# Performance work log

Hardware: AMD Instinct MI355X
Metric: run time of the kernel (lower is better)

Reference implementation:

```python
import jax, jax.numpy as jnp
import numpy as np

N, E, D, R, B = 30000, 100000, 200, 100, 50
BN_EPS = 1e-5


def setup_inputs() -> dict:
    key = jax.random.key(0)
    ks = list(jax.random.split(key, 26))
    s = 1.0 / np.sqrt(D)  # xavier-ish scale
    lin = lambda k: jax.random.normal(k, (D, D), jnp.float32) * s
    bias = lambda k: jax.random.normal(k, (D,), jnp.float32) * 0.01
    return {
        "n_in_feats": jax.random.normal(ks[0], (N, D), jnp.float32),
        "r_feats": jax.random.normal(ks[1], (R, D), jnp.float32),
        "norm": jax.random.uniform(ks[2], (E, 1), jnp.float32),
        "loop_rel": jax.random.normal(ks[3], (1, D), jnp.float32) * s,
        "relation_att": jax.random.normal(ks[4], (B, D, D), jnp.float32) * s,
        "w_comp": jax.random.normal(ks[5], (R, B), jnp.float32) * 0.115,
        "wO_w": lin(ks[6]), "wO_b": bias(ks[7]),
        "wI_w": lin(ks[8]), "wI_b": bias(ks[9]),
        "wS_w": lin(ks[10]), "wS_b": bias(ks[11]),
        "wR_w": lin(ks[12]), "wR_b": bias(ks[13]),
        "k_w": lin(ks[14]), "k_b": bias(ks[15]),
        "q_w": lin(ks[16]), "q_b": bias(ks[17]),
        "v_w": lin(ks[18]), "v_b": bias(ks[19]),
        "bn_gamma": jnp.ones((D,), jnp.float32),
        "bn_beta": jnp.zeros((D,), jnp.float32),
        "src": jax.random.randint(ks[20], (E,), 0, N),
        "dst": jax.random.randint(ks[21], (E,), 0, N),
        "etype": jax.random.randint(ks[22], (E,), 0, R),
        "in_mask": jax.random.randint(ks[23], (E,), 0, 2, dtype=jnp.int32),
    }


def reference(n_in_feats, r_feats, norm, loop_rel, relation_att, w_comp,
              wO_w, wO_b, wI_w, wI_b, wS_w, wS_b, wR_w, wR_b,
              k_w, k_b, q_w, q_b, v_w, v_b, bn_gamma, bn_beta,
              src, dst, etype, in_mask):
    r_all = jnp.concatenate([r_feats, loop_rel], axis=0)      # [R+1, D]
    x_src = n_in_feats[src]                                   # [E, D]
    x_dst = n_in_feats[dst]                                   # [E, D]

    # composition (comp_fn='sub') + in/out projections.
    # NOTE: in the original source new_comp_h is computed and stored on edges
    # but never consumed downstream (dead w.r.t. outputs); kept for fidelity.
    comp_h = x_src - r_all[etype] * norm                      # [E, D]
    new_comp_h = jnp.where(in_mask[:, None] > 0,
                           comp_h @ wI_w.T + wI_b,
                           comp_h @ wO_w.T + wO_b)            # [E, D] (unused)

    # per-edge k/q/v from endpoint node features
    k = x_src @ k_w.T + k_b                                   # [E, D]
    q = x_dst @ q_w.T + q_b                                   # [E, D]
    v = x_src @ v_w.T + v_b                                   # [E, D]

    # basis-decomposed relational attention: att_e = k_e^T (sum_b w_comp[t_e,b] A_b) q_e
    # scan over bases avoids materializing [E, B, D]
    def per_basis(c, A_b):
        return c, jnp.sum((k @ A_b) * q, axis=-1)             # [E]
    _, s = jax.lax.scan(per_basis, None, relation_att)        # [B, E]
    att = jnp.sum(w_comp[etype] * s.T, axis=-1)               # [E]

    # segment softmax over destination nodes (== DGL mailbox softmax)
    m = jax.ops.segment_max(att, dst, num_segments=N)
    m = jnp.where(jnp.isfinite(m), m, 0.0)                    # empty segments -> 0
    ex = jnp.exp(att - m[dst])
    denom = jax.ops.segment_sum(ex, dst, num_segments=N)
    wts = ex / jnp.maximum(denom[dst], 1e-30)                 # [E]
    agg = jax.ops.segment_sum(wts[:, None] * v, dst, num_segments=N)  # [N, D]

    # self-loop branch + merge (dropout is identity at eval)
    comp_h_s = n_in_feats - loop_rel                          # sub with loop relation
    n_out = ((comp_h_s @ wS_w.T + wS_b) + agg) * (1.0 / 3.0)

    # BatchNorm1d in training mode (batch statistics, biased variance)
    mean = jnp.mean(n_out, axis=0)
    var = jnp.var(n_out, axis=0)
    n_out = bn_gamma * (n_out - mean) * jax.lax.rsqrt(var + BN_EPS) + bn_beta
    n_out = jnp.tanh(n_out)

    r_out = (r_all @ wR_w.T + wR_b)[:-1]                      # [R, D]
    return n_out, r_out
```

## Files before the change

### kernel.cpp

```cpp
#include <hip/hip_runtime.h>
#include <hip/hip_bf16.h>
#include <math.h>

typedef __hip_bfloat16 bf16;
typedef __attribute__((ext_vector_type(8))) short short8;
typedef __attribute__((ext_vector_type(4))) float f32x4;

#define NN 30000
#define NE 100000
#define DD 200
#define NR 100
#define NB 50
#define NDIM (NN*DD)
#define MAXCH 1664
#define NBLK 391
#define SEGB 40

#define KP 224
#define NCOLP 896
#define MIP 208

#define O_K      0
#define O_V      6240000
#define O_QH     12240000
#define O_QL     15600000
#define O_MH     18960000
#define O_ML     21289600
#define O_WTH    23619200
#define O_WTL    23719552
#define O_B800   23819904
#define O_ATT    23820704
#define O_SUM    23920704
#define O_SSQ    23920904
#define O_CNT    23921104
#define O_OFFS   23921204
#define O_CUR    23921305
#define O_CHOFF  23921405
#define O_NCH    23921506
#define O_CHT    23921507
#define O_CHS    23923171
#define O_CHL    23924835
#define O_EIDX   23926499
#define O_CNTD   24026499
#define O_OFFD   24056499
#define O_CURD   24086500
#define O_EIDXD  24116500
#define O_BH     24216500

__device__ __forceinline__ float cvt(float x) { return x; }
__device__ __forceinline__ float cvt(bf16 x) { return __bfloat162float(x); }
__device__ __forceinline__ short f2bf(float f) {
    union { float f; unsigned u; } x; x.f = f;
    unsigned r = x.u + 0x7FFFu + ((x.u >> 16) & 1u);
    return (short)(r >> 16);
}
__device__ __forceinline__ float bf2f(short b) {
    union { unsigned u; float f; } x; x.u = ((unsigned)(unsigned short)b) << 16;
    return x.f;
}
__device__ __forceinline__ bool bfmode(const void* gam) {
    return *(const unsigned*)gam != 0x3F800000u;
}

__global__ void k_init(float* __restrict__ ws) {
    int g = blockIdx.x * 256 + threadIdx.x;
    int* wi = (int*)ws;
    if (g < NN) wi[O_CNTD + g] = 0;
    if (g < DD) { ws[O_SUM + g] = 0.f; ws[O_SSQ + g] = 0.f; }
}

template <typename T>
__device__ __forceinline__ void prep_body(float* __restrict__ ws,
        const T* kw, const T* qw, const T* vw, const T* sw,
        const T* kb, const T* qb, const T* vb, const T* sb, const T* lr, int g) {
    if (g < NCOLP * KP) {
        int c = g / KP, k = g % KP;
        float val = 0.f;
        if (c < 800 && k < DD) {
            int m = c / 200, cc = c - m * 200;
            const T* w = (m == 0) ? kw : (m == 1) ? qw : (m == 2) ? vw : sw;
            val = cvt(w[cc * 200 + k]);
        }
        short hi = f2bf(val);
        short lo = f2bf(val - bf2f(hi));
        ((short*)(ws + O_WTH))[g] = hi;
        ((short*)(ws + O_WTL))[g] = lo;
    } else if (g < NCOLP * KP + 800) {
        int c = g - NCOLP * KP;
        int m = c / 200, cc = c - m * 200;
        float v;
        if (m == 0) v = cvt(kb[cc]);
        else if (m == 1) v = cvt(qb[cc]);
        else if (m == 2) v = cvt(vb[cc]);
        else {
            float acc = cvt(sb[cc]);
            for (int j = 0; j < DD; j++) acc -= cvt(lr[j]) * cvt(sw[cc * 200 + j]);
            v = acc;
        }
        ws[O_B800 + c] = v;
    }
}
__global__ void k_prep(float* __restrict__ ws,
                       const void* kw, const void* qw, const void* vw, const void* sw,
                       const void* kb, const void* qb, const void* vb, const void* sb,
                       const void* lr, const void* gam) {
    int g = blockIdx.x * 256 + threadIdx.x;
    if (bfmode(gam))
        prep_body(ws, (const bf16*)kw, (const bf16*)qw, (const bf16*)vw, (const bf16*)sw,
                  (const bf16*)kb, (const bf16*)qb, (const bf16*)vb, (const bf16*)sb,
                  (const bf16*)lr, g);
    else
        prep_body(ws, (const float*)kw, (const float*)qw, (const float*)vw, (const float*)sw,
                  (const float*)kb, (const float*)qb, (const float*)vb, (const float*)sb,
                  (const float*)lr, g);
}

template <typename T>
__device__ __forceinline__ void compmt_body(float* __restrict__ ws, const T* A, const T* wc,
                                            float* wl, int tid, int bx, int by) {
    for (int idx = tid; idx < NR * NB; idx += 256) wl[idx] = cvt(wc[idx]);
    __syncthreads();
    int x = bx * 256 + tid;
    int i = x / KP, j = x - i * KP;
    bool valid = (i < DD) && (j < DD);
    float a[NB];
    if (valid) {
        #pragma unroll
        for (int b = 0; b < NB; b++) a[b] = cvt(A[b * 40000 + i * 200 + j]);
    } else {
        #pragma unroll
        for (int b = 0; b < NB; b++) a[b] = 0.f;
    }
    short* mh = (short*)(ws + O_MH);
    short* ml = (short*)(ws + O_ML);
    int t0 = by * 25;
    for (int t = t0; t < t0 + 25; t++) {
        float acc = 0.f;
        #pragma unroll
        for (int b = 0; b < NB; b++) acc = fmaf(wl[t * NB + b], a[b], acc);
        short hi = f2bf(acc);
        short lo = f2bf(acc - bf2f(hi));
        mh[(size_t)t * (MIP * KP) + x] = hi;
        ml[(size_t)t * (MIP * KP) + x] = lo;
    }
}
__global__ void k_compmt(float* __restrict__ ws, const void* A, const void* wc,
                         const void* gam) {
    __shared__ float wl[NR * NB];
    if (bfmode(gam)) compmt_body(ws, (const bf16*)A, (const bf16*)wc, wl,
                                 threadIdx.x, blockIdx.x, blockIdx.y);
    else             compmt_body(ws, (const float*)A, (const float*)wc, wl,
                                 threadIdx.x, blockIdx.x, blockIdx.y);
}

__global__ void k_hist(float* __restrict__ ws, const int* __restrict__ ety,
                       const int* __restrict__ dst) {
    __shared__ int lh[NR];
    int tid = threadIdx.x;
    if (tid < NR) lh[tid] = 0;
    __syncthreads();
    int e = blockIdx.x * 256 + tid;
    int* wi = (int*)ws;
    if (e < NE) {
        atomicAdd(&lh[ety[e]], 1);
        atomicAdd(&wi[O_CNTD + dst[e]], 1);
    }
    __syncthreads();
    if (tid < NR) wi[O_BH + blockIdx.x * NR + tid] = lh[tid];
}

__global__ void k_scans(float* __restrict__ ws) {
    __shared__ int part[1024];
    __shared__ int segsum[10 * NR];
    __shared__ int cntL[NR];
    __shared__ int offsL[NR + 1];
    int* wi = (int*)ws;
    int tid = threadIdx.x;
    int t = tid % NR, seg = tid / NR;

    if (tid < 1000) {
        int b0 = seg * SEGB;
        int b1 = min(NBLK, b0 + SEGB);
        int s = 0;
        for (int b = b0; b < b1; b++) s += wi[O_BH + b * NR + t];
        segsum[seg * NR + t] = s;
    }
    __syncthreads();
    if (tid < NR) {
        int s = 0;
        #pragma unroll
        for (int g = 0; g < 10; g++) s += segsum[g * NR + tid];
        cntL[tid] = s;
        wi[O_CNT + tid] = s;
    }
    __syncthreads();
    if (tid == 0) {
        int run = 0, chrun = 0;
        for (int ty = 0; ty < NR; ty++) {
            offsL[ty] = run;
            wi[O_OFFS + ty] = run;
            wi[O_CHOFF + ty] = chrun;
            run += cntL[ty];
            chrun += (cntL[ty] + 63) >> 6;
        }
        offsL[NR] = run;
        wi[O_OFFS + NR] = run;
        wi[O_CHOFF + NR] = chrun;
        wi[O_NCH] = chrun;
    }
    __syncthreads();
    if (tid < 1000) {
        int base = offsL[t];
        for (int g = 0; g < seg; g++) base += segsum[g * NR + t];
        int b0 = seg * SEGB;
        int nb = min(NBLK - b0, SEGB);
        int cvals[SEGB];
        #pragma unroll
        for (int i = 0; i < SEGB; i++)
            if (i < nb) cvals[i] = wi[O_BH + (b0 + i) * NR + t];
        #pragma unroll
        for (int i = 0; i < SEGB; i++) {
            if (i < nb) {
                wi[O_BH + (b0 + i) * NR + t] = base;
                base += cvals[i];
            }
        }
    }
    __syncthreads();
    int nch = wi[O_NCH];
    for (int c = tid; c < nch; c += 1024) {
        int lo = 0, hi = NR;
        while (hi - lo > 1) {
            int mid = (lo + hi) >> 1;
            if (wi[O_CHOFF + mid] <= c) lo = mid; else hi = mid;
        }
        int local = c - wi[O_CHOFF + lo];
        wi[O_CHT + c] = lo;
        wi[O_CHS + c] = offsL[lo] + local * 64;
        wi[O_CHL + c] = min(64, cntL[lo] - local * 64);
    }
    __syncthreads();
    int i0 = tid * 30;
    int s = 0;
    for (int u = 0; u < 30; u++) { int i = i0 + u; if (i < NN) s += wi[O_CNTD + i]; }
    part[tid] = s;
    __syncthreads();
    for (int off = 1; off < 1024; off <<= 1) {
        int v = 0;
        if (tid >= off) v = part[tid - off];
        __syncthreads();
        part[tid] += v;
        __syncthreads();
    }
    int run = part[tid] - s;
    for (int u = 0; u < 30; u++) {
        int i = i0 + u;
        if (i < NN) {
            wi[O_OFFD + i] = run;
            wi[O_CURD + i] = run;
            run += wi[O_CNTD + i];
        }
    }
    if (tid == 1023) wi[O_OFFD + NN] = part[1023];
}

__global__ void k_scatter(float* __restrict__ ws, const int* __restrict__ ety,
                          const int* __restrict__ dst) {
    __shared__ int lcnt[NR];
    int tid = threadIdx.x;
    if (tid < NR) lcnt[tid] = 0;
    __syncthreads();
    int e = blockIdx.x * 256 + tid;
    int* wi = (int*)ws;
    if (e < NE) {
        int t = ety[e];
        int r = atomicAdd(&lcnt[t], 1);
        wi[O_EIDX + wi[O_BH + blockIdx.x * NR + t] + r] = e;
        int p2 = atomicAdd(&wi[O_CURD + dst[e]], 1);
        wi[O_EIDXD + p2] = e;
    }
}

__global__ __launch_bounds__(256, 3) void k_ngemm(float* __restrict__ ws, const float* __restrict__ X,
                                                  float* __restrict__ outAgg) {
    __shared__ short Bh[128 * 40];
    __shared__ short Bl[128 * 40];
    int tid = threadIdx.x;
    int wid = tid >> 6, lane = tid & 63;
    int l16 = lane & 15, quad = lane >> 4;
    int r0 = blockIdx.x * 64 + wid * 16;
    int c0 = blockIdx.y * 128;
    bool needLo = (c0 < 400);

    const float* xr = X + (size_t)min(r0 + l16, NN - 1) * DD;
    short8 ah[7], al[7];
    #pragma unroll
    for (int kk = 0; kk < 7; kk++) {
        int k0 = kk * 32 + quad * 8;
        float v[8] = {0.f, 0.f, 0.f, 0.f, 0.f, 0.f, 0.f, 0.f};
        if (k0 < DD) {
            float4 v0 = *(const float4*)(xr + k0);
            float4 v1 = *(const float4*)(xr + k0 + 4);
            v[0] = v0.x; v[1] = v0.y; v[2] = v0.z; v[3] = v0.w;
            v[4] = v1.x; v[5] = v1.y; v[6] = v1.z; v[7] = v1.w;
        }
        #pragma unroll
        for (int j = 0; j < 8; j++) {
            short hi = f2bf(v[j]);
            ah[kk][j] = hi;
            al[kk][j] = f2bf(v[j] - bf2f(hi));
        }
    }

    const short* WTH = (const short*)(ws + O_WTH);
    const short* WTL = (const short*)(ws + O_WTL);
    f32x4 acc[8] = {};
    for (int kk = 0; kk < 7; kk++) {
        {
            int n = tid >> 1;
            int ko = (tid & 1) * 16;
            size_t off = (size_t)(c0 + n) * KP + kk * 32 + ko;
            *(float4*)&Bh[n * 40 + ko]     = *(const float4*)(WTH + off);
            *(float4*)&Bh[n * 40 + ko + 8] = *(const float4*)(WTH + off + 8);
            if (needLo) {
                *(float4*)&Bl[n * 40 + ko]     = *(const float4*)(WTL + off);
                *(float4*)&Bl[n * 40 + ko + 8] = *(const float4*)(WTL + off + 8);
            }
        }
        __syncthreads();
        #pragma unroll
        for (int nt = 0; nt < 8; nt++) {
            int ro = (nt * 16 + l16) * 40 + quad * 8;
            short8 bh = *(const short8*)&Bh[ro];
            acc[nt] = __builtin_amdgcn_mfma_f32_16x16x32_bf16(ah[kk], bh, acc[nt], 0, 0, 0);
            acc[nt] = __builtin_amdgcn_mfma_f32_16x16x32_bf16(al[kk], bh, acc[nt], 0, 0, 0);
            if (c0 + nt * 16 < 400) {
                short8 bl = *(const short8*)&Bl[ro];
                acc[nt] = __builtin_amdgcn_mfma_f32_16x16x32_bf16(ah[kk], bl, acc[nt], 0, 0, 0);
            }
        }
        __syncthreads();
    }

    const float* B800 = ws + O_B800;
    short* QHs = (short*)(ws + O_QH);
    short* QLs = (short*)(ws + O_QL);
    float* Kp = ws + O_K;
    short* VpS = (short*)(ws + O_V);
    int rowBase = r0 + quad * 4;
    #pragma unroll
    for (int nt = 0; nt < 8; nt++) {
        int col = c0 + nt * 16 + l16;
        if (col < 800) {
            int m = (col >= 600) ? 3 : (col >= 400) ? 2 : (col >= 200) ? 1 : 0;
            int cc = col - m * 200;
            float bias = B800[col];
            #pragma unroll
            for (int reg = 0; reg < 4; reg++) {
                int row = rowBase + reg;
                if (row >= NN) continue;
                float v = acc[nt][reg] + bias;
                if (m == 0) Kp[(size_t)row * 208 + cc] = v;
                else if (m == 1) {
                    short hi = f2bf(v);
                    short lo = f2bf(v - bf2f(hi));
                    QHs[(size_t)row * 224 + cc] = hi;
                    QLs[(size_t)row * 224 + cc] = lo;
                } else if (m == 2) VpS[(size_t)row * 200 + cc] = f2bf(v);
                else outAgg[(size_t)row * 200 + cc] = v;
            }
        } else {
            int p = col - 800;
            #pragma unroll
            for (int reg = 0; reg < 4; reg++) {
                int row = rowBase + reg;
                if (row >= NN) continue;
                if (p < 8)        Kp[(size_t)row * 208 + 200 + p] = 0.f;
                else if (p < 32)  QHs[(size_t)row * 224 + 192 + p] = 0;
                else if (p < 56)  QLs[(size_t)row * 224 + 168 + p] = 0;
            }
        }
    }
}

template <int MTN>
__device__ __forceinline__ void attn_core(
        const short* (&qh)[4], const short* (&ql)[4],
        const short* mhb, const short* mlb,
        const float* __restrict__ Kp, const int* __restrict__ srcv, const int (&eId)[4],
        int mt0, int quad, float (&part)[4]) {
    f32x4 acc[4][MTN];
    #pragma unroll
    for (int et = 0; et < 4; et++)
        #pragma unroll
        for (int ml = 0; ml < MTN; ml++) acc[et][ml] = (f32x4){0.f, 0.f, 0.f, 0.f};

    #pragma unroll
    for (int kc = 0; kc < 7; kc++) {
        int kk = kc * 32;
        short8 bh[4], bl[4];
        #pragma unroll
        for (int et = 0; et < 4; et++) {
            bh[et] = *(const short8*)(qh[et] + kk);
            bl[et] = *(const short8*)(ql[et] + kk);
        }
        #pragma unroll
        for (int ml = 0; ml < MTN; ml++) {
            short8 ah = *(const short8*)(mhb + (size_t)ml * 16 * KP + kk);
            short8 al = *(const short8*)(mlb + (size_t)ml * 16 * KP + kk);
            #pragma unroll
            for (int et = 0; et < 4; et++) {
                acc[et][ml] = __builtin_amdgcn_mfma_f32_16x16x32_bf16(ah, bh[et], acc[et][ml], 0, 0, 0);
                acc[et][ml] = __builtin_amdgcn_mfma_f32_16x16x32_bf16(ah, bl[et], acc[et][ml], 0, 0, 0);
                acc[et][ml] = __builtin_amdgcn_mfma_f32_16x16x32_bf16(al, bh[et], acc[et][ml], 0, 0, 0);
            }
        }
    }

    #pragma unroll
    for (int et = 0; et < 4; et++) {
        const float* krow = Kp + (size_t)srcv[eId[et]] * 208 + mt0 * 16 + quad * 4;
        float p = 0.f;
        #pragma unroll
        for (int ml = 0; ml < MTN; ml++) {
            float4 kv = *(const float4*)(krow + ml * 16);
            p = fmaf(kv.x, acc[et][ml][0], p);
            p = fmaf(kv.y, acc[et][ml][1], p);
            p = fmaf(kv.z, acc[et][ml][2], p);
            p = fmaf(kv.w, acc[et][ml][3], p);
        }
        part[et] = p;
    }
}

__global__ __launch_bounds__(256) void k_attn(const int* __restrict__ cht, const int* __restrict__ chs,
                                              const int* __restrict__ chl, const int* __restrict__ nchp,
                                              const int* __restrict__ eidx, const int* __restrict__ srcv,
                                              const int* __restrict__ dstv,
                                              const float* __restrict__ Kp,
                                              const short* __restrict__ QH, const short* __restrict__ QL,
                                              const short* __restrict__ MH, const short* __restrict__ ML,
                                              float* __restrict__ attOut) {
    __shared__ float attp[4 * 64];
    int b = blockIdx.x;
    int b2 = (b & 7) * 208 + (b >> 3);
    if (b2 >= nchp[0]) return;
    int tid = threadIdx.x;
    int wid = tid >> 6, lane = tid & 63;
    int l16 = lane & 15, quad = lane >> 4;
    int t   = __builtin_amdgcn_readfirstlane(cht[b2]);
    int s0  = __builtin_amdgcn_readfirstlane(chs[b2]);
    int len = __builtin_amdgcn_readfirstlane(chl[b2]);
    int mt0 = wid * 3;

    int eId[4];
    const short* qh[4];
    const short* ql[4];
    #pragma unroll
    for (int et = 0; et < 4; et++) {
        eId[et] = eidx[s0 + min(et * 16 + l16, len - 1)];
        int dn = dstv[eId[et]];
        qh[et] = QH + (size_t)dn * KP + quad * 8;
        ql[et] = QL + (size_t)dn * KP + quad * 8;
    }
    const short* mhb = MH + (size_t)t * (MIP * KP) + (size_t)(mt0 * 16 + l16) * KP + quad * 8;
    const short* mlb = ML + (size_t)t * (MIP * KP) + (size_t)(mt0 * 16 + l16) * KP + quad * 8;

    float part[4];
    if (wid == 3) attn_core<4>(qh, ql, mhb, mlb, Kp, srcv, eId, mt0, quad, part);
    else          attn_core<3>(qh, ql, mhb, mlb, Kp, srcv, eId, mt0, quad, part);

    #pragma unroll
    for (int et = 0; et < 4; et++) {
        float v = part[et];
        v += __shfl_xor(v, 16);
        v += __shfl_xor(v, 32);
        if (quad == 0) attp[wid * 64 + et * 16 + l16] = v;
    }
    __syncthreads();
    if (tid < 64 && tid < len) {
        attOut[eidx[s0 + tid]] = attp[tid] + attp[64 + tid] + attp[128 + tid] + attp[192 + tid];
    }
}

__global__ __launch_bounds__(256) void k_nodeagg(const int* __restrict__ offd, const int* __restrict__ eidxd,
                                                 const int* __restrict__ src, const float* __restrict__ att,
                                                 const short* __restrict__ V, float* __restrict__ agg) {
    int wav = threadIdx.x >> 6, lane = threadIdx.x & 63;
    int n = blockIdx.x * 4 + wav;
    if (n >= NN) return;
    int o0 = offd[n], o1 = offd[n + 1];
    float* arow = agg + (size_t)n * 200;
    if (o1 > o0) {
        float a0 = arow[lane], a1 = arow[64 + lane], a2 = arow[128 + lane];
        float a3 = (lane < 8) ? arow[192 + lane] : 0.f;
        float m = -INFINITY;
        for (int p = o0; p < o1; p++) m = fmaxf(m, att[eidxd[p]]);
        float den = 0.f;
        for (int p = o0; p < o1; p++) den += expf(att[eidxd[p]] - m);
        float rden = 1.f / fmaxf(den, 1e-30f);
        for (int p = o0; p < o1; p++) {
            int e = eidxd[p];
            float w = expf(att[e] - m) * rden;
            const short* vrow = V + (size_t)src[e] * 200;
            a0 = fmaf(w, bf2f(vrow[lane]), a0);
            a1 = fmaf(w, bf2f(vrow[64 + lane]), a1);
            a2 = fmaf(w, bf2f(vrow[128 + lane]), a2);
            if (lane < 8) a3 = fmaf(w, bf2f(vrow[192 + lane]), a3);
        }
        arow[lane] = a0; arow[64 + lane] = a1; arow[128 + lane] = a2;
        if (lane < 8) arow[192 + lane] = a3;
    }
}

__global__ void k_bnstats(const float* __restrict__ agg, float* __restrict__ sum,
                          float* __restrict__ ssq) {
    int col = threadIdx.x;
    if (col >= DD) return;
    int r0 = blockIdx.x * 120;
    float s = 0.f, q = 0.f;
    for (int r = 0; r < 120; r++) {
        float x = agg[(size_t)(r0 + r) * 200 + col] * (1.f / 3.f);
        s += x;
        q = fmaf(x, x, q);
    }
    atomicAdd(&sum[col], s);
    atomicAdd(&ssq[col], q);
}

template <typename T>
__device__ __forceinline__ void bnfin_body(float* sum, float* ssq, const T* gamma, const T* beta, int d) {
    float mean = sum[d] * (1.f / NN);
    float var = ssq[d] * (1.f / NN) - mean * mean;
    float inv = rsqrtf(var + 1e-5f);
    float scale = cvt(gamma[d]) * inv;
    float shift = cvt(beta[d]) - mean * scale;
    sum[d] = scale;
    ssq[d] = shift;
}
__global__ void k_bnfin(float* __restrict__ sum, float* __restrict__ ssq,
                        const void* gamma, const void* beta) {
    int d = threadIdx.x;
    if (d >= DD) return;
    if (bfmode(gamma)) bnfin_body(sum, ssq, (const bf16*)gamma, (const bf16*)beta, d);
    else               bnfin_body(sum, ssq, (const float*)gamma, (const float*)beta, d);
}

template <typename T>
__device__ __forceinline__ void rout_body(const T* rf, const T* wr, const T* wrb,
                                          float* out, int g) {
    int r = g / 200, d = g - r * 200;
    float acc = cvt(wrb[d]);
    const T* xr = rf + r * 200;
    const T* wrow = wr + d * 200;
    for (int k = 0; k < 200; k++) acc = fmaf(cvt(xr[k]), cvt(wrow[k]), acc);
    out[NDIM + g] = acc;
}
__global__ void k_finish(const float* __restrict__ agg, const float* __restrict__ scale,
                         const float* __restrict__ shift,
                         const void* rf, const void* wr, const void* wrb,
                         float* __restrict__ out, const void* gam) {
    int bx = blockIdx.x;
    if (bx < 23438) {
        int g = bx * 256 + threadIdx.x;
        if (g >= NDIM) return;
        int d = g % 200;
        float x = agg[g] * (1.f / 3.f);
        float y = fmaf(x, scale[d], shift[d]);
        out[g] = tanhf(y);
    } else {
        int g = (bx - 23438) * 256 + threadIdx.x;
        if (g >= NR * DD) return;
        if (bfmode(gam)) rout_body((const bf16*)rf, (const bf16*)wr, (const bf16*)wrb, out, g);
        else             rout_body((const float*)rf, (const float*)wr, (const float*)wrb, out, g);
    }
}

extern "C" void kernel_launch(void* const* d_in, const int* in_sizes, int n_in,
                              void* d_out, int out_size, void* d_ws, size_t ws_size,
                              hipStream_t stream) {
    (void)in_sizes; (void)n_in; (void)out_size; (void)ws_size;
    const void* X   = d_in[0];
    const void* RF  = d_in[1];
    const void* LR  = d_in[3];
    const void* A   = d_in[4];
    const void* WC  = d_in[5];
    const void* SW  = d_in[10]; const void* SB = d_in[11];
    const void* RW  = d_in[12]; const void* RB = d_in[13];
    const void* KW  = d_in[14]; const void* KB = d_in[15];
    const void* QW  = d_in[16]; const void* QB = d_in[17];
    const void* VW  = d_in[18]; const void* VB = d_in[19];
    const void* GAM = d_in[20]; const void* BET = d_in[21];
    const int* src = (const int*)d_in[22];
    const int* dst = (const int*)d_in[23];
    const int* ety = (const int*)d_in[24];
    float* ws = (float*)d_ws;
    int* wsi = (int*)d_ws;
    float* out = (float*)d_out;

    k_init<<<118, 256, 0, stream>>>(ws);
    k_prep<<<788, 256, 0, stream>>>(ws, KW, QW, VW, SW, KB, QB, VB, SB, LR, GAM);
    k_compmt<<<dim3(182, 4), 256, 0, stream>>>(ws, A, WC, GAM);
    k_hist<<<NBLK, 256, 0, stream>>>(ws, ety, dst);
    k_scans<<<1, 1024, 0, stream>>>(ws);
    k_scatter<<<NBLK, 256, 0, stream>>>(ws, ety, dst);
    k_ngemm<<<dim3(469, 7), 256, 0, stream>>>(ws, (const float*)X, out);
    k_attn<<<MAXCH, 256, 0, stream>>>(wsi + O_CHT, wsi + O_CHS, wsi + O_CHL, wsi + O_NCH,
                                      wsi + O_EIDX, src, dst,
                                      ws + O_K,
                                      (const short*)(ws + O_QH), (const short*)(ws + O_QL),
                                      (const short*)(ws + O_MH), (const short*)(ws + O_ML),
                                      ws + O_ATT);
    k_nodeagg<<<7500, 256, 0, stream>>>(wsi + O_OFFD, wsi + O_EIDXD, src,
                                        ws + O_ATT, (const short*)(ws + O_V), out);
    k_bnstats<<<250, 256, 0, stream>>>(out, ws + O_SUM, ws + O_SSQ);
    k_bnfin<<<1, 256, 0, stream>>>(ws + O_SUM, ws + O_SSQ, GAM, BET);
    k_finish<<<23517, 256, 0, stream>>>(out, ws + O_SUM, ws + O_SSQ, RF, RW, RB, out, GAM);
}
```

Before: 473.3 us.

## Interleave hi/lo bf16 planes, fuse setup kernels, dst-ordered attention buffers

```diff
diff --git a/kernel.cpp b/kernel.cpp
--- a/kernel.cpp
+++ b/kernel.cpp
@@ -19,33 +19,32 @@
 #define KP 224
 #define NCOLP 896
 #define MIP 208
+#define MTS 93184
 
 #define O_K      0
 #define O_V      6240000
-#define O_QH     12240000
-#define O_QL     15600000
-#define O_MH     18960000
-#define O_ML     21289600
-#define O_WTH    23619200
-#define O_WTL    23719552
-#define O_B800   23819904
-#define O_ATT    23820704
-#define O_SUM    23920704
-#define O_SSQ    23920904
-#define O_CNT    23921104
-#define O_OFFS   23921204
-#define O_CUR    23921305
-#define O_CHOFF  23921405
-#define O_NCH    23921506
-#define O_CHT    23921507
-#define O_CHS    23923171
-#define O_CHL    23924835
-#define O_EIDX   23926499
-#define O_CNTD   24026499
-#define O_OFFD   24056499
-#define O_CURD   24086500
-#define O_EIDXD  24116500
-#define O_BH     24216500
+#define O_QI     9240000
+#define O_MI     15960000
+#define O_WTH    20619200
+#define O_WTL    20719552
+#define O_B800   20819904
+#define O_ATTD   20820704
+#define O_SUM    20920704
+#define O_SSQ    20920904
+#define O_CNT    20921104
+#define O_OFFS   20921204
+#define O_CHOFF  20921305
+#define O_NCH    20921406
+#define O_CHT    20921407
+#define O_CHS    20923071
+#define O_CHL    20924735
+#define O_EIDX   20926399
+#define O_CNTD   21026399
+#define O_OFFD   21056399
+#define O_CURD   21086400
+#define O_RNKD   21116400
+#define O_SRCD   21216400
+#define O_BH     21316400
 
 __device__ __forceinline__ float cvt(float x) { return x; }
 __device__ __forceinline__ float cvt(bf16 x) { return __bfloat162float(x); }
@@ -60,13 +59,6 @@
 }
 __device__ __forceinline__ bool bfmode(const void* gam) {
     return *(const unsigned*)gam != 0x3F800000u;
-}
-
-__global__ void k_init(float* __restrict__ ws) {
-    int g = blockIdx.x * 256 + threadIdx.x;
-    int* wi = (int*)ws;
-    if (g < NN) wi[O_CNTD + g] = 0;
-    if (g < DD) { ws[O_SUM + g] = 0.f; ws[O_SSQ + g] = 0.f; }
 }
 
 template <typename T>
@@ -100,20 +92,6 @@
         ws[O_B800 + c] = v;
     }
 }
-__global__ void k_prep(float* __restrict__ ws,
-                       const void* kw, const void* qw, const void* vw, const void* sw,
-                       const void* kb, const void* qb, const void* vb, const void* sb,
-                       const void* lr, const void* gam) {
-    int g = blockIdx.x * 256 + threadIdx.x;
-    if (bfmode(gam))
-        prep_body(ws, (const bf16*)kw, (const bf16*)qw, (const bf16*)vw, (const bf16*)sw,
-                  (const bf16*)kb, (const bf16*)qb, (const bf16*)vb, (const bf16*)sb,
-                  (const bf16*)lr, g);
-    else
-        prep_body(ws, (const float*)kw, (const float*)qw, (const float*)vw, (const float*)sw,
-                  (const float*)kb, (const float*)qb, (const float*)vb, (const float*)sb,
-                  (const float*)lr, g);
-}
 
 template <typename T>
 __device__ __forceinline__ void compmt_body(float* __restrict__ ws, const T* A, const T* wc,
@@ -131,8 +109,9 @@
         #pragma unroll
         for (int b = 0; b < NB; b++) a[b] = 0.f;
     }
-    short* mh = (short*)(ws + O_MH);
-    short* ml = (short*)(ws + O_ML);
+    short* mi = (short*)(ws + O_MI);
+    int kc = j >> 5, jj = j & 31, qd = jj >> 3, pos = jj & 7;
+    size_t slot = (size_t)i * 448 + (kc * 4 + qd) * 16 + pos;
     int t0 = by * 25;
     for (int t = t0; t < t0 + 25; t++) {
         float acc = 0.f;
@@ -140,17 +119,46 @@
         for (int b = 0; b < NB; b++) acc = fmaf(wl[t * NB + b], a[b], acc);
         short hi = f2bf(acc);
         short lo = f2bf(acc - bf2f(hi));
-        mh[(size_t)t * (MIP * KP) + x] = hi;
-        ml[(size_t)t * (MIP * KP) + x] = lo;
-    }
-}
-__global__ void k_compmt(float* __restrict__ ws, const void* A, const void* wc,
-                         const void* gam) {
+        size_t off = (size_t)t * MTS + slot;
+        mi[off] = hi;
+        mi[off + 8] = lo;
+    }
+}
+
+template <typename T>
+__device__ __forceinline__ void setup_body(float* __restrict__ ws,
+        const T* A, const T* wc,
+        const T* kw, const T* qw, const T* vw, const T* sw,
+        const T* kb, const T* qb, const T* vb, const T* sb, const T* lr,
+        float* wl, int bidx, int tid) {
+    if (bidx < 118) {
+        int g = bidx * 256 + tid;
+        int* wi = (int*)ws;
+        if (g < NN) wi[O_CNTD + g] = 0;
+        if (g < DD) { ws[O_SUM + g] = 0.f; ws[O_SSQ + g] = 0.f; }
+    } else if (bidx < 906) {
+        int g = (bidx - 118) * 256 + tid;
+        prep_body(ws, kw, qw, vw, sw, kb, qb, vb, sb, lr, g);
+    } else {
+        int idx = bidx - 906;
+        compmt_body(ws, A, wc, wl, tid, idx % 182, idx / 182);
+    }
+}
+__global__ void k_setup(float* __restrict__ ws, const void* A, const void* wc,
+                        const void* kw, const void* qw, const void* vw, const void* sw,
+                        const void* kb, const void* qb, const void* vb, const void* sb,
+                        const void* lr, const void* gam) {
     __shared__ float wl[NR * NB];
-    if (bfmode(gam)) compmt_body(ws, (const bf16*)A, (const bf16*)wc, wl,
-                                 threadIdx.x, blockIdx.x, blockIdx.y);
-    else             compmt_body(ws, (const float*)A, (const float*)wc, wl,
-                                 threadIdx.x, blockIdx.x, blockIdx.y);
+    if (bfmode(gam))
+        setup_body(ws, (const bf16*)A, (const bf16*)wc,
+                   (const bf16*)kw, (const bf16*)qw, (const bf16*)vw, (const bf16*)sw,
+                   (const bf16*)kb, (const bf16*)qb, (const bf16*)vb, (const bf16*)sb,
+                   (const bf16*)lr, wl, blockIdx.x, threadIdx.x);
+    else
+        setup_body(ws, (const float*)A, (const float*)wc,
+                   (const float*)kw, (const float*)qw, (const float*)vw, (const float*)sw,
+                   (const float*)kb, (const float*)qb, (const float*)vb, (const float*)sb,
+                   (const float*)lr, wl, blockIdx.x, threadIdx.x);
 }
 
 __global__ void k_hist(float* __restrict__ ws, const int* __restrict__ ety,
@@ -265,7 +273,7 @@
 }
 
 __global__ void k_scatter(float* __restrict__ ws, const int* __restrict__ ety,
-                          const int* __restrict__ dst) {
+                          const int* __restrict__ dst, const int* __restrict__ src) {
     __shared__ int lcnt[NR];
     int tid = threadIdx.x;
     if (tid < NR) lcnt[tid] = 0;
@@ -277,7 +285,8 @@
         int r = atomicAdd(&lcnt[t], 1);
         wi[O_EIDX + wi[O_BH + blockIdx.x * NR + t] + r] = e;
         int p2 = atomicAdd(&wi[O_CURD + dst[e]], 1);
-        wi[O_EIDXD + p2] = e;
+        wi[O_RNKD + e] = p2;
+        wi[O_SRCD + p2] = src[e];
     }
 }
 
@@ -289,8 +298,6 @@
     int wid = tid >> 6, lane = tid & 63;
     int l16 = lane & 15, quad = lane >> 4;
     int r0 = blockIdx.x * 64 + wid * 16;
-    int c0 = blockIdx.y * 128;
-    bool needLo = (c0 < 400);
 
     const float* xr = X + (size_t)min(r0 + l16, NN - 1) * DD;
     short8 ah[7], al[7];
@@ -314,70 +321,84 @@
 
     const short* WTH = (const short*)(ws + O_WTH);
     const short* WTL = (const short*)(ws + O_WTL);
-    f32x4 acc[8] = {};
-    for (int kk = 0; kk < 7; kk++) {
-        {
-            int n = tid >> 1;
-            int ko = (tid & 1) * 16;
-            size_t off = (size_t)(c0 + n) * KP + kk * 32 + ko;
-            *(float4*)&Bh[n * 40 + ko]     = *(const float4*)(WTH + off);
-            *(float4*)&Bh[n * 40 + ko + 8] = *(const float4*)(WTH + off + 8);
-            if (needLo) {
-                *(float4*)&Bl[n * 40 + ko]     = *(const float4*)(WTL + off);
-                *(float4*)&Bl[n * 40 + ko + 8] = *(const float4*)(WTL + off + 8);
-            }
-        }
-        __syncthreads();
-        #pragma unroll
-        for (int nt = 0; nt < 8; nt++) {
-            int ro = (nt * 16 + l16) * 40 + quad * 8;
-            short8 bh = *(const short8*)&Bh[ro];
-            acc[nt] = __builtin_amdgcn_mfma_f32_16x16x32_bf16(ah[kk], bh, acc[nt], 0, 0, 0);
-            acc[nt] = __builtin_amdgcn_mfma_f32_16x16x32_bf16(al[kk], bh, acc[nt], 0, 0, 0);
-            if (c0 + nt * 16 < 400) {
-                short8 bl = *(const short8*)&Bl[ro];
-                acc[nt] = __builtin_amdgcn_mfma_f32_16x16x32_bf16(ah[kk], bl, acc[nt], 0, 0, 0);
-            }
-        }
-        __syncthreads();
-    }
-
     const float* B800 = ws + O_B800;
-    short* QHs = (short*)(ws + O_QH);
-    short* QLs = (short*)(ws + O_QL);
+    short* QIs = (short*)(ws + O_QI);
     float* Kp = ws + O_K;
     short* VpS = (short*)(ws + O_V);
-    int rowBase = r0 + quad * 4;
-    #pragma unroll
-    for (int nt = 0; nt < 8; nt++) {
-        int col = c0 + nt * 16 + l16;
-        if (col < 800) {
-            int m = (col >= 600) ? 3 : (col >= 400) ? 2 : (col >= 200) ? 1 : 0;
-            int cc = col - m * 200;
-            float bias = B800[col];
+    int ct0 = (blockIdx.y == 0) ? 0 : 4;
+    int ct1 = (blockIdx.y == 0) ? 4 : 7;
+
+    for (int ct = ct0; ct < ct1; ct++) {
+        int c0 = ct * 128;
+        bool needLo = (c0 < 400);
+        f32x4 acc[8] = {};
+        #pragma unroll
+        for (int kk = 0; kk < 7; kk++) {
+            {
+                int n = tid >> 1;
+                int ko = (tid & 1) * 16;
+                size_t off = (size_t)(c0 + n) * KP + kk * 32 + ko;
+                *(float4*)&Bh[n * 40 + ko]     = *(const float4*)(WTH + off);
+                *(float4*)&Bh[n * 40 + ko + 8] = *(const float4*)(WTH + off + 8);
+                if (needLo) {
+                    *(float4*)&Bl[n * 40 + ko]     = *(const float4*)(WTL + off);
+                    *(float4*)&Bl[n * 40 + ko + 8] = *(const float4*)(WTL + off + 8);
+                }
+            }
+            __syncthreads();
             #pragma unroll
-            for (int reg = 0; reg < 4; reg++) {
-                int row = rowBase + reg;
-                if (row >= NN) continue;
-                float v = acc[nt][reg] + bias;
-                if (m == 0) Kp[(size_t)row * 208 + cc] = v;
-                else if (m == 1) {
-                    short hi = f2bf(v);
-                    short lo = f2bf(v - bf2f(hi));
-                    QHs[(size_t)row * 224 + cc] = hi;
-                    QLs[(size_t)row * 224 + cc] = lo;
-                } else if (m == 2) VpS[(size_t)row * 200 + cc] = f2bf(v);
-                else outAgg[(size_t)row * 200 + cc] = v;
+            for (int nt = 0; nt < 8; nt++) {
+                int ro = (nt * 16 + l16) * 40 + quad * 8;
+                short8 bh = *(const short8*)&Bh[ro];
+                acc[nt] = __builtin_amdgcn_mfma_f32_16x16x32_bf16(ah[kk], bh, acc[nt], 0, 0, 0);
+                acc[nt] = __builtin_amdgcn_mfma_f32_16x16x32_bf16(al[kk], bh, acc[nt], 0, 0, 0);
+                if (c0 + nt * 16 < 400) {
+                    short8 bl = *(const short8*)&Bl[ro];
+                    acc[nt] = __builtin_amdgcn_mfma_f32_16x16x32_bf16(ah[kk], bl, acc[nt], 0, 0, 0);
+                }
             }
-        } else {
-            int p = col - 800;
-            #pragma unroll
-            for (int reg = 0; reg < 4; reg++) {
-                int row = rowBase + reg;
-                if (row >= NN) continue;
-                if (p < 8)        Kp[(size_t)row * 208 + 200 + p] = 0.f;
-                else if (p < 32)  QHs[(size_t)row * 224 + 192 + p] = 0;
-                else if (p < 56)  QLs[(size_t)row * 224 + 168 + p] = 0;
+            __syncthreads();
+        }
+
+        int rowBase = r0 + quad * 4;
+        #pragma unroll
+        for (int nt = 0; nt < 8; nt++) {
+            int col = c0 + nt * 16 + l16;
+            if (col < 800) {
+                int m = (col >= 600) ? 3 : (col >= 400) ? 2 : (col >= 200) ? 1 : 0;
+                int cc = col - m * 200;
+                float bias = B800[col];
+                #pragma unroll
+                for (int reg = 0; reg < 4; reg++) {
+                    int row = rowBase + reg;
+                    if (row >= NN) continue;
+                    float v = acc[nt][reg] + bias;
+                    if (m == 0) Kp[(size_t)row * 208 + cc] = v;
+                    else if (m == 1) {
+                        short hi = f2bf(v);
+                        short lo = f2bf(v - bf2f(hi));
+                        int kc = cc >> 5, jj = cc & 31, qd = jj >> 3, pos = jj & 7;
+                        size_t qoff = (size_t)row * 448 + (kc * 4 + qd) * 16 + pos;
+                        QIs[qoff] = hi;
+                        QIs[qoff + 8] = lo;
+                    } else if (m == 2) VpS[(size_t)row * 200 + cc] = f2bf(v);
+                    else outAgg[(size_t)row * 200 + cc] = v;
+                }
+            } else {
+                int p = col - 800;
+                #pragma unroll
+                for (int reg = 0; reg < 4; reg++) {
+                    int row = rowBase + reg;
+                    if (row >= NN) continue;
+                    if (p < 8) Kp[(size_t)row * 208 + 200 + p] = 0.f;
+                    else if (p < 56) {
+                        int h = p - 8;
+                        int plane = h / 24;
+                        int k = 200 + h - plane * 24;
+                        int kc = k >> 5, jj = k & 31, qd = jj >> 3, pos = jj & 7;
+                        QIs[(size_t)row * 448 + (kc * 4 + qd) * 16 + pos + plane * 8] = 0;
+                    }
+                }
             }
         }
     }
@@ -385,8 +406,7 @@
 
 template <int MTN>
 __device__ __forceinline__ void attn_core(
-        const short* (&qh)[4], const short* (&ql)[4],
-        const short* mhb, const short* mlb,
+        const short* (&qi)[4], const short* mib,
         const float* __restrict__ Kp, const int* __restrict__ srcv, const int (&eId)[4],
         int mt0, int quad, float (&part)[4]) {
     f32x4 acc[4][MTN];
@@ -397,17 +417,18 @@
 
     #pragma unroll
     for (int kc = 0; kc < 7; kc++) {
-        int kk = kc * 32;
         short8 bh[4], bl[4];
         #pragma unroll
         for (int et = 0; et < 4; et++) {
-            bh[et] = *(const short8*)(qh[et] + kk);
-            bl[et] = *(const short8*)(ql[et] + kk);
+            const short* qp = qi[et] + kc * 64;
+            bh[et] = *(const short8*)(qp);
+            bl[et] = *(const short8*)(qp + 8);
         }
         #pragma unroll
         for (int ml = 0; ml < MTN; ml++) {
-            short8 ah = *(const short8*)(mhb + (size_t)ml * 16 * KP + kk);
-            short8 al = *(const short8*)(mlb + (size_t)ml * 16 * KP + kk);
+            const short* mp = mib + ml * 7168 + kc * 64;
+            short8 ah = *(const short8*)(mp);
+            short8 al = *(const short8*)(mp + 8);
             #pragma unroll
             for (int et = 0; et < 4; et++) {
                 acc[et][ml] = __builtin_amdgcn_mfma_f32_16x16x32_bf16(ah, bh[et], acc[et][ml], 0, 0, 0);
@@ -438,9 +459,8 @@
                                               const int* __restrict__ eidx, const int* __restrict__ srcv,
                                               const int* __restrict__ dstv,
                                               const float* __restrict__ Kp,
-                                              const short* __restrict__ QH, const short* __restrict__ QL,
-                                              const short* __restrict__ MH, const short* __restrict__ ML,
-                                              float* __restrict__ attOut) {
+                                              const short* __restrict__ QI, const short* __restrict__ MI,
+                                              const int* __restrict__ rnkd, float* __restrict__ attd) {
     __shared__ float attp[4 * 64];
     int b = blockIdx.x;
     int b2 = (b & 7) * 208 + (b >> 3);
@@ -454,21 +474,17 @@
     int mt0 = wid * 3;
 
     int eId[4];
-    const short* qh[4];
-    const short* ql[4];
+    const short* qi[4];
     #pragma unroll
     for (int et = 0; et < 4; et++) {
         eId[et] = eidx[s0 + min(et * 16 + l16, len - 1)];
-        int dn = dstv[eId[et]];
-        qh[et] = QH + (size_t)dn * KP + quad * 8;
-        ql[et] = QL + (size_t)dn * KP + quad * 8;
-    }
-    const short* mhb = MH + (size_t)t * (MIP * KP) + (size_t)(mt0 * 16 + l16) * KP + quad * 8;
-    const short* mlb = ML + (size_t)t * (MIP * KP) + (size_t)(mt0 * 16 + l16) * KP + quad * 8;
+        qi[et] = QI + (size_t)dstv[eId[et]] * 448 + quad * 16;
+    }
+    const short* mib = MI + (size_t)t * MTS + (size_t)(mt0 * 16 + l16) * 448 + quad * 16;
 
     float part[4];
-    if (wid == 3) attn_core<4>(qh, ql, mhb, mlb, Kp, srcv, eId, mt0, quad, part);
-    else          attn_core<3>(qh, ql, mhb, mlb, Kp, srcv, eId, mt0, quad, part);
+    if (wid == 3) attn_core<4>(qi, mib, Kp, srcv, eId, mt0, quad, part);
+    else          attn_core<3>(qi, mib, Kp, srcv, eId, mt0, quad, part);
 
     #pragma unroll
     for (int et = 0; et < 4; et++) {
@@ -479,12 +495,13 @@
     }
     __syncthreads();
     if (tid < 64 && tid < len) {
-        attOut[eidx[s0 + tid]] = attp[tid] + attp[64 + tid] + attp[128 + tid] + attp[192 + tid];
-    }
-}
-
-__global__ __launch_bounds__(256) void k_nodeagg(const int* __restrict__ offd, const int* __restrict__ eidxd,
-                                                 const int* __restrict__ src, const float* __restrict__ att,
+        int e2 = eidx[s0 + tid];
+        attd[rnkd[e2]] = attp[tid] + attp[64 + tid] + attp[128 + tid] + attp[192 + tid];
+    }
+}
+
+__global__ __launch_bounds__(256) void k_nodeagg(const int* __restrict__ offd, const int* __restrict__ srcd,
+                                                 const float* __restrict__ attd,
                                                  const short* __restrict__ V, float* __restrict__ agg) {
     int wav = threadIdx.x >> 6, lane = threadIdx.x & 63;
     int n = blockIdx.x * 4 + wav;
@@ -495,14 +512,13 @@
         float a0 = arow[lane], a1 = arow[64 + lane], a2 = arow[128 + lane];
         float a3 = (lane < 8) ? arow[192 + lane] : 0.f;
         float m = -INFINITY;
-        for (int p = o0; p < o1; p++) m = fmaxf(m, att[eidxd[p]]);
+        for (int p = o0; p < o1; p++) m = fmaxf(m, attd[p]);
         float den = 0.f;
-        for (int p = o0; p < o1; p++) den += expf(att[eidxd[p]] - m);
+        for (int p = o0; p < o1; p++) den += expf(attd[p] - m);
         float rden = 1.f / fmaxf(den, 1e-30f);
         for (int p = o0; p < o1; p++) {
-            int e = eidxd[p];
-            float w = expf(att[e] - m) * rden;
-            const short* vrow = V + (size_t)src[e] * 200;
+            float w = expf(attd[p] - m) * rden;
+            const short* vrow = V + (size_t)srcd[p] * 200;
             a0 = fmaf(w, bf2f(vrow[lane]), a0);
             a1 = fmaf(w, bf2f(vrow[64 + lane]), a1);
             a2 = fmaf(w, bf2f(vrow[128 + lane]), a2);
@@ -598,21 +614,18 @@
     int* wsi = (int*)d_ws;
     float* out = (float*)d_out;
 
-    k_init<<<118, 256, 0, stream>>>(ws);
-    k_prep<<<788, 256, 0, stream>>>(ws, KW, QW, VW, SW, KB, QB, VB, SB, LR, GAM);
-    k_compmt<<<dim3(182, 4), 256, 0, stream>>>(ws, A, WC, GAM);
+    k_setup<<<1634, 256, 0, stream>>>(ws, A, WC, KW, QW, VW, SW, KB, QB, VB, SB, LR, GAM);
     k_hist<<<NBLK, 256, 0, stream>>>(ws, ety, dst);
     k_scans<<<1, 1024, 0, stream>>>(ws);
-    k_scatter<<<NBLK, 256, 0, stream>>>(ws, ety, dst);
-    k_ngemm<<<dim3(469, 7), 256, 0, stream>>>(ws, (const float*)X, out);
+    k_scatter<<<NBLK, 256, 0, stream>>>(ws, ety, dst, src);
+    k_ngemm<<<dim3(469, 2), 256, 0, stream>>>(ws, (const float*)X, out);
     k_attn<<<MAXCH, 256, 0, stream>>>(wsi + O_CHT, wsi + O_CHS, wsi + O_CHL, wsi + O_NCH,
                                       wsi + O_EIDX, src, dst,
                                       ws + O_K,
-                                      (const short*)(ws + O_QH), (const short*)(ws + O_QL),
-                                      (const short*)(ws + O_MH), (const short*)(ws + O_ML),
-                                      ws + O_ATT);
-    k_nodeagg<<<7500, 256, 0, stream>>>(wsi + O_OFFD, wsi + O_EIDXD, src,
-                                        ws + O_ATT, (const short*)(ws + O_V), out);
+                                      (const short*)(ws + O_QI), (const short*)(ws + O_MI),
+                                      wsi + O_RNKD, ws + O_ATTD);
+    k_nodeagg<<<7500, 256, 0, stream>>>(wsi + O_OFFD, wsi + O_SRCD,
+                                        ws + O_ATTD, (const short*)(ws + O_V), out);
     k_bnstats<<<250, 256, 0, stream>>>(out, ws + O_SUM, ws + O_SSQ);
     k_bnfin<<<1, 256, 0, stream>>>(ws + O_SUM, ws + O_SSQ, GAM, BET);
     k_finish<<<23517, 256, 0, stream>>>(out, ws + O_SUM, ws + O_SSQ, RF, RW, RB, out, GAM);
```

New measurement: 500.2 us. 5.7% more time.
